# Performance work log

Measured on AMD Instinct MI355X. Metric: run time of the kernel, lower is better.

## Reference

```python
import jax, jax.numpy as jnp
import numpy as np

B, T, C, H = 4, 2048, 1024, 64  # batch, seq, embedding_size, head_size

def setup_inputs() -> dict:
    key = jax.random.key(0)
    k0, k1, k2, k3 = jax.random.split(key, 4)
    scale = 0.02
    return {
        "x":  jax.random.normal(k0, (B, T, C), dtype=jnp.float32),
        "Wq": jax.random.normal(k1, (H, C), dtype=jnp.float32) * scale,
        "Wk": jax.random.normal(k2, (H, C), dtype=jnp.float32) * scale,
        "Wv": jax.random.normal(k3, (H, C), dtype=jnp.float32) * scale,
    }

def reference(x, Wq, Wk, Wv):
    # Linear(bias=False): y = x @ W^T
    q = jnp.einsum('btc,hc->bth', x, Wq)
    k = jnp.einsum('btc,hc->bth', x, Wk)
    v = jnp.einsum('btc,hc->bth', x, Wv)
    # NOTE: original scales by embedding_size C**-0.5, not head_size
    wei = jnp.einsum('bth,bsh->bts', q, k) * (x.shape[-1] ** -0.5)
    t = x.shape[1]
    causal_mask = jnp.tril(jnp.ones((t, t), dtype=bool))  # [T, T]
    wei = jnp.where(causal_mask, wei, -jnp.inf)
    wei = jax.nn.softmax(wei, axis=-1)
    # dropout = 0.0 -> identity (eval mode)
    out = jnp.einsum('bts,bsh->bth', wei, v)
    return out
```

## Files before the change

### kernel.cpp

```cpp
#include <hip/hip_runtime.h>
#include <hip/hip_bf16.h>

typedef unsigned short u16;
typedef __attribute__((ext_vector_type(8))) __bf16 bf16x8;
typedef __attribute__((ext_vector_type(4))) float f32x4;

#define B_ 4
#define T_ 2048
#define C_ 1024
#define H_ 64
#define NSEG 8

__device__ __forceinline__ u16 f2bf(float f) {
    union { __hip_bfloat16 h; u16 u; } cv;
    cv.h = __float2bfloat16(f);
    return cv.u;
}

__device__ __forceinline__ bf16x8 cvt8r(float4 f0, float4 f1) {
    union { u16 h[8]; bf16x8 v; } ua;
    ua.h[0] = f2bf(f0.x); ua.h[1] = f2bf(f0.y);
    ua.h[2] = f2bf(f0.z); ua.h[3] = f2bf(f0.w);
    ua.h[4] = f2bf(f1.x); ua.h[5] = f2bf(f1.y);
    ua.h[6] = f2bf(f1.z); ua.h[7] = f2bf(f1.w);
    return ua.v;
}

__device__ __forceinline__ void gll16(const void* g, void* l) {
    __builtin_amdgcn_global_load_lds(
        (const __attribute__((address_space(1))) void*)g,
        (__attribute__((address_space(3))) void*)l, 16, 0, 0);
}

__global__ __launch_bounds__(256) void wpack(
    const float* __restrict__ wq, const float* __restrict__ wk,
    const float* __restrict__ wv, u16* __restrict__ wP)
{
    int u    = blockIdx.x * 256 + threadIdx.x;
    int ln   = u & 63;
    int frag = u >> 6;
    int ksg  = frag & 31;
    int j16  = frag >> 5;
    int n    = j16 * 16 + (ln & 15);
    int kb   = ksg * 32 + (ln >> 4) * 8;
    const float* src = (n < 64) ? (wq + (size_t)n * C_)
                     : (n < 128) ? (wk + (size_t)(n - 64) * C_)
                                 : (wv + (size_t)(n - 128) * C_);
    float4 f0 = *(const float4*)(src + kb);
    float4 f1 = *(const float4*)(src + kb + 4);
    *(bf16x8*)(wP + (size_t)u * 8) = cvt8r(f0, f1);
}

__global__ __launch_bounds__(512) void qkv(
    const float* __restrict__ x, const u16* __restrict__ wP,
    u16* __restrict__ qP, u16* __restrict__ kP, u16* __restrict__ vP)
{
    __shared__ __align__(16) char smem[32768];

    const int tid = threadIdx.x;
    const int ln  = tid & 63;
    const int w   = tid >> 6;
    const int m0  = blockIdx.x * 32;

    const int lr = ln & 15;
    const int g  = ln >> 4;
    const int ms = w >> 2;
    const int nh = w & 3;

    f32x4 acc[3] = {};

    const int xrow = w * 4 + (ln >> 4);
    const int xc   = (ln & 15) ^ (xrow & 7);

#define STAGE(BUF, KC)                                                     \
    gll16(x + (size_t)(m0 + xrow) * C_ + (KC) * 64 + xc * 4,               \
          smem + (BUF) * 8192 + w * 1024)

    STAGE(0, 0);
    STAGE(1, 1);
    STAGE(2, 2);

    const int ra  = ms * 16 + lr;
    const int rsw = ra & 7;
    const u16* wbase = wP + (size_t)(nh * 3) * 32 * 64 * 8;

    #pragma unroll
    for (int kc = 0; kc < 16; ++kc) {
        if (kc == 0)       asm volatile("s_waitcnt vmcnt(2)"  ::: "memory");
        else if (kc == 1)  asm volatile("s_waitcnt vmcnt(8)"  ::: "memory");
        else if (kc <= 13) asm volatile("s_waitcnt vmcnt(14)" ::: "memory");
        else if (kc == 14) asm volatile("s_waitcnt vmcnt(13)" ::: "memory");
        else               asm volatile("s_waitcnt vmcnt(12)" ::: "memory");
        __builtin_amdgcn_s_barrier();
        __builtin_amdgcn_sched_barrier(0);

        const char* rb = smem + (kc & 3) * 8192;

        bf16x8 a[2];
        #pragma unroll
        for (int ks = 0; ks < 2; ++ks) {
            int c0 = ks * 8 + g * 2;
            float4 fa = *(const float4*)(rb + ra * 256 + ((c0       ^ rsw) << 4));
            float4 fb = *(const float4*)(rb + ra * 256 + (((c0 + 1) ^ rsw) << 4));
            a[ks] = cvt8r(fa, fb);
        }

        #pragma unroll
        for (int j = 0; j < 3; ++j) {
            #pragma unroll
            for (int ks = 0; ks < 2; ++ks) {
                size_t fragofs = ((size_t)(j * 32 + kc * 2 + ks) * 64 + ln) * 8;
                bf16x8 b = *(const bf16x8*)(wbase + fragofs);
                acc[j] = __builtin_amdgcn_mfma_f32_16x16x32_bf16(a[ks], b, acc[j], 0, 0, 0);
            }
        }

        if (kc < 13) STAGE((kc + 3) & 3, kc + 3);
    }
#undef STAGE

    __syncthreads();

    float* tile = (float*)smem;
    #pragma unroll
    for (int j = 0; j < 3; ++j)
        #pragma unroll
        for (int i = 0; i < 4; ++i)
            tile[(ms * 16 + g * 4 + i) * 201 + nh * 48 + j * 16 + lr] = acc[j][i];
    __syncthreads();

    for (int uu = tid; uu < 768; uu += 512) {
        const int ln2 = uu & 63;
        const int lr2 = ln2 & 15;
        const int g2  = ln2 >> 4;
        if (uu < 512) {
            const int isK = uu >> 8;
            const int rem = uu & 255;
            const int u   = rem >> 7;
            const int ks  = (rem >> 6) & 1;
            const float* src = tile + (u * 16 + lr2) * 201 + isK * 64 + ks * 32 + g2 * 8;
            float4 f0 = *(const float4*)src;
            float4 f1 = *(const float4*)(src + 4);
            bf16x8 val = cvt8r(f0, f1);
            u16* dst = (isK ? kP : qP)
                     + ((size_t)(((m0 >> 4) + u) * 2 + ks) * 64 + ln2) * 8;
            *(bf16x8*)dst = val;
        } else {
            const int rem = uu - 512;
            const int jf  = rem >> 6;
            union { u16 h[8]; bf16x8 v; } ua;
            #pragma unroll
            for (int e = 0; e < 8; ++e)
                ua.h[e] = f2bf(tile[(g2 * 8 + e) * 201 + 128 + jf * 16 + lr2]);
            u16* dst = vP + ((size_t)((m0 >> 5) * 4 + jf) * 64 + ln2) * 8;
            *(bf16x8*)dst = ua.v;
        }
    }
}

__global__ __launch_bounds__(512) void attn(
    const u16* __restrict__ qP, const u16* __restrict__ kP,
    const u16* __restrict__ vP, float* __restrict__ out)
{
    __shared__ __align__(16) char shm[34816];

    const int tid  = threadIdx.x;
    const int lane = tid & 63;
    const int seg  = tid >> 6;
    const int tix  = blockIdx.x;
    const int b    = tix & 3;
    const int qt   = 127 - (tix >> 2);
    const int q0   = qt * 16;

    const int lr = lane & 15;
    const int g  = lane >> 4;
    const int lk = g * 8;

    const int nch = (qt >> 2) + 1;
    const int L   = (nch + NSEG - 1) >> 3;
    const int c0  = seg * L;
    const int c1  = min(nch, c0 + L);

    f32x4 oacc[4] = {};
    float mrow[4], lrow[4];
    #pragma unroll
    for (int i = 0; i < 4; ++i) { mrow[i] = -1e30f; lrow[i] = 0.f; }

    if (c0 < c1) {
        bf16x8 aq[2];
        #pragma unroll
        for (int ks = 0; ks < 2; ++ks)
            aq[ks] = *(const bf16x8*)(qP + ((size_t)((b * 128 + qt) * 2 + ks) * 64 + lane) * 8);

        u16* myps = (u16*)shm + seg * 1152;

        for (int jc = c0; jc < c1; ++jc) {
            const int kv0 = jc << 6;

            bf16x8 bk[8];
            #pragma unroll
            for (int jf = 0; jf < 4; ++jf)
                #pragma unroll
                for (int ks = 0; ks < 2; ++ks)
                    bk[jf * 2 + ks] = *(const bf16x8*)(kP +
                        ((size_t)((b * 128 + (kv0 >> 4) + jf) * 2 + ks) * 64 + lane) * 8);

            f32x4 sacc[4] = {};
            #pragma unroll
            for (int jf = 0; jf < 4; ++jf)
                #pragma unroll
                for (int ks = 0; ks < 2; ++ks)
                    sacc[jf] = __builtin_amdgcn_mfma_f32_16x16x32_bf16(aq[ks], bk[jf * 2 + ks], sacc[jf], 0, 0, 0);

            bf16x8 bv[8];
            #pragma unroll
            for (int ks2 = 0; ks2 < 2; ++ks2)
                #pragma unroll
                for (int jf = 0; jf < 4; ++jf)
                    bv[jf * 2 + ks2] = *(const bf16x8*)(vP +
                        ((size_t)((b * 64 + (kv0 >> 5) + ks2) * 4 + jf) * 64 + lane) * 8);

            const bool full = (kv0 + 63 <= q0);
            #pragma unroll
            for (int jf = 0; jf < 4; ++jf) {
                int col = kv0 + jf * 16 + lr;
                #pragma unroll
                for (int i = 0; i < 4; ++i) {
                    int row = q0 + g * 4 + i;
                    float val = sacc[jf][i] * 0.03125f;
                    sacc[jf][i] = (full || col <= row) ? val : -1e30f;
                }
            }

            float pnew[4][4];
            #pragma unroll
            for (int i = 0; i < 4; ++i) {
                float mx = fmaxf(fmaxf(sacc[0][i], sacc[1][i]), fmaxf(sacc[2][i], sacc[3][i]));
                mx = fmaxf(mx, __shfl_xor(mx, 1));
                mx = fmaxf(mx, __shfl_xor(mx, 2));
                mx = fmaxf(mx, __shfl_xor(mx, 4));
                mx = fmaxf(mx, __shfl_xor(mx, 8));
                float mnew = fmaxf(mrow[i], mx);
                float corr = __expf(mrow[i] - mnew);
                float rs = 0.f;
                #pragma unroll
                for (int jf = 0; jf < 4; ++jf) {
                    float p = __expf(sacc[jf][i] - mnew);
                    pnew[jf][i] = p;
                    rs += p;
                }
                rs += __shfl_xor(rs, 1);
                rs += __shfl_xor(rs, 2);
                rs += __shfl_xor(rs, 4);
                rs += __shfl_xor(rs, 8);
                lrow[i] = lrow[i] * corr + rs;
                mrow[i] = mnew;
                #pragma unroll
                for (int jf = 0; jf < 4; ++jf) oacc[jf][i] *= corr;
            }

            #pragma unroll
            for (int jf = 0; jf < 4; ++jf)
                #pragma unroll
                for (int i = 0; i < 4; ++i)
                    myps[(g * 4 + i) * 72 + jf * 16 + lr] = f2bf(pnew[jf][i]);

            #pragma unroll
            for (int ks2 = 0; ks2 < 2; ++ks2) {
                bf16x8 ap = *(const bf16x8*)(myps + lr * 72 + ks2 * 32 + lk);
                #pragma unroll
                for (int jf = 0; jf < 4; ++jf)
                    oacc[jf] = __builtin_amdgcn_mfma_f32_16x16x32_bf16(ap, bv[jf * 2 + ks2], oacc[jf], 0, 0, 0);
            }
        }
    }

    __syncthreads();

    float* part = (float*)shm;
    float* mlp  = part + 8 * 16 * 66;

    if (c0 >= c1) {
        if (lr == 0)
            #pragma unroll
            for (int i = 0; i < 4; ++i) {
                mlp[(seg * 16 + g * 4 + i) * 2]     = -1e30f;
                mlp[(seg * 16 + g * 4 + i) * 2 + 1] = 0.f;
            }
    } else {
        #pragma unroll
        for (int jf = 0; jf < 4; ++jf)
            #pragma unroll
            for (int i = 0; i < 4; ++i)
                part[(seg * 16 + g * 4 + i) * 66 + jf * 16 + lr] = oacc[jf][i];
        if (lr == 0)
            #pragma unroll
            for (int i = 0; i < 4; ++i) {
                mlp[(seg * 16 + g * 4 + i) * 2]     = mrow[i];
                mlp[(seg * 16 + g * 4 + i) * 2 + 1] = lrow[i];
            }
    }

    __syncthreads();

    if (tid < 256) {
        const int row = tid >> 4;
        const int p   = tid & 15;

        float m2[NSEG], l2[NSEG];
        #pragma unroll
        for (int s = 0; s < NSEG; ++s) {
            m2[s] = mlp[(s * 16 + row) * 2];
            l2[s] = mlp[(s * 16 + row) * 2 + 1];
        }
        float M = m2[0];
        #pragma unroll
        for (int s = 1; s < NSEG; ++s) M = fmaxf(M, m2[s]);

        float a0 = 0.f, a1 = 0.f, a2 = 0.f, a3 = 0.f, Lsum = 0.f;
        #pragma unroll
        for (int s = 0; s < NSEG; ++s) {
            if (l2[s] != 0.f) {
                float wgt = __expf(m2[s] - M);
                Lsum += l2[s] * wgt;
                const float* pp = part + (s * 16 + row) * 66 + p * 4;
                a0 += wgt * pp[0];
                a1 += wgt * pp[1];
                a2 += wgt * pp[2];
                a3 += wgt * pp[3];
            }
        }
        float inv = 1.f / Lsum;
        float4 r; r.x = a0 * inv; r.y = a1 * inv; r.z = a2 * inv; r.w = a3 * inv;
        *(float4*)(out + ((size_t)b * T_ + qt * 16 + row) * H_ + p * 4) = r;
    }
}

extern "C" void kernel_launch(void* const* d_in, const int* in_sizes, int n_in,
                              void* d_out, int out_size, void* d_ws, size_t ws_size,
                              hipStream_t stream) {
    const float* x  = (const float*)d_in[0];
    const float* wq = (const float*)d_in[1];
    const float* wk = (const float*)d_in[2];
    const float* wv = (const float*)d_in[3];

    u16* qPws = (u16*)d_ws;
    u16* kPws = qPws + (size_t)B_ * T_ * H_;
    u16* vPws = kPws + (size_t)B_ * T_ * H_;
    u16* wPws = vPws + (size_t)B_ * T_ * H_;

    wpack<<<96, 256, 0, stream>>>(wq, wk, wv, wPws);
    qkv<<<256, 512, 0, stream>>>(x, wPws, qPws, kPws, vPws);
    attn<<<512, 512, 0, stream>>>(qPws, kPws, vPws, (float*)d_out);
}
```

Before: 37.88 us.

## Fuse QKV projection and attention into one kernel with grid-wide barrier

Merges the qkv and attn kernels into a single persistent kernel of 256 blocks. Blocks first compute their QKV tile, then synchronize through a global atomic counter barrier (reset in wpack), and each block then processes two attention tiles (tix and 511-tix) to balance the causal workload. This removes one kernel launch and its tail/drain gap, but adds a spin barrier that assumes all 256 blocks are co-resident and halves the number of attention blocks in flight.

```diff
diff --git a/kernel.cpp b/kernel.cpp
--- a/kernel.cpp
+++ b/kernel.cpp
@@ -10,6 +10,7 @@
 #define C_ 1024
 #define H_ 64
 #define NSEG 8
+#define GRID 256
 
 __device__ __forceinline__ u16 f2bf(float f) {
     union { __hip_bfloat16 h; u16 u; } cv;
@@ -34,8 +35,10 @@
 
 __global__ __launch_bounds__(256) void wpack(
     const float* __restrict__ wq, const float* __restrict__ wk,
-    const float* __restrict__ wv, u16* __restrict__ wP)
+    const float* __restrict__ wv, u16* __restrict__ wP,
+    unsigned* __restrict__ bar)
 {
+    if (blockIdx.x == 0 && threadIdx.x == 0) bar[0] = 0;
     int u    = blockIdx.x * 256 + threadIdx.x;
     int ln   = u & 63;
     int frag = u >> 6;
@@ -51,288 +54,296 @@
     *(bf16x8*)(wP + (size_t)u * 8) = cvt8r(f0, f1);
 }
 
-__global__ __launch_bounds__(512) void qkv(
+__global__ __launch_bounds__(512) void fused(
     const float* __restrict__ x, const u16* __restrict__ wP,
-    u16* __restrict__ qP, u16* __restrict__ kP, u16* __restrict__ vP)
+    u16* __restrict__ qP, u16* __restrict__ kP, u16* __restrict__ vP,
+    float* __restrict__ out, unsigned* __restrict__ bar)
 {
-    __shared__ __align__(16) char smem[32768];
+    __shared__ __align__(16) char shm[34816];
 
     const int tid = threadIdx.x;
     const int ln  = tid & 63;
     const int w   = tid >> 6;
-    const int m0  = blockIdx.x * 32;
-
-    const int lr = ln & 15;
-    const int g  = ln >> 4;
-    const int ms = w >> 2;
-    const int nh = w & 3;
-
-    f32x4 acc[3] = {};
-
-    const int xrow = w * 4 + (ln >> 4);
-    const int xc   = (ln & 15) ^ (xrow & 7);
+    const int lr  = ln & 15;
+    const int g   = ln >> 4;
+    const int lk  = g * 8;
+
+    {
+        char* smem = shm;
+        const int m0 = blockIdx.x * 32;
+        const int ms = w >> 2;
+        const int nh = w & 3;
+
+        f32x4 acc[3] = {};
+
+        const int xrow = w * 4 + (ln >> 4);
+        const int xc   = (ln & 15) ^ (xrow & 7);
 
 #define STAGE(BUF, KC)                                                     \
     gll16(x + (size_t)(m0 + xrow) * C_ + (KC) * 64 + xc * 4,               \
           smem + (BUF) * 8192 + w * 1024)
 
-    STAGE(0, 0);
-    STAGE(1, 1);
-    STAGE(2, 2);
-
-    const int ra  = ms * 16 + lr;
-    const int rsw = ra & 7;
-    const u16* wbase = wP + (size_t)(nh * 3) * 32 * 64 * 8;
-
-    #pragma unroll
-    for (int kc = 0; kc < 16; ++kc) {
-        if (kc == 0)       asm volatile("s_waitcnt vmcnt(2)"  ::: "memory");
-        else if (kc == 1)  asm volatile("s_waitcnt vmcnt(8)"  ::: "memory");
-        else if (kc <= 13) asm volatile("s_waitcnt vmcnt(14)" ::: "memory");
-        else if (kc == 14) asm volatile("s_waitcnt vmcnt(13)" ::: "memory");
-        else               asm volatile("s_waitcnt vmcnt(12)" ::: "memory");
-        __builtin_amdgcn_s_barrier();
-        __builtin_amdgcn_sched_barrier(0);
-
-        const char* rb = smem + (kc & 3) * 8192;
-
-        bf16x8 a[2];
+        STAGE(0, 0);
+        STAGE(1, 1);
+        STAGE(2, 2);
+
+        const int ra  = ms * 16 + lr;
+        const int rsw = ra & 7;
+        const u16* wbase = wP + (size_t)(nh * 3) * 32 * 64 * 8;
+
         #pragma unroll
-        for (int ks = 0; ks < 2; ++ks) {
-            int c0 = ks * 8 + g * 2;
-            float4 fa = *(const float4*)(rb + ra * 256 + ((c0       ^ rsw) << 4));
-            float4 fb = *(const float4*)(rb + ra * 256 + (((c0 + 1) ^ rsw) << 4));
-            a[ks] = cvt8r(fa, fb);
-        }
-
+        for (int kc = 0; kc < 16; ++kc) {
+            if (kc == 0)       asm volatile("s_waitcnt vmcnt(2)"  ::: "memory");
+            else if (kc == 1)  asm volatile("s_waitcnt vmcnt(8)"  ::: "memory");
+            else if (kc <= 13) asm volatile("s_waitcnt vmcnt(14)" ::: "memory");
+            else if (kc == 14) asm volatile("s_waitcnt vmcnt(13)" ::: "memory");
+            else               asm volatile("s_waitcnt vmcnt(12)" ::: "memory");
+            __builtin_amdgcn_s_barrier();
+            __builtin_amdgcn_sched_barrier(0);
+
+            const char* rb = smem + (kc & 3) * 8192;
+
+            bf16x8 a[2];
+            #pragma unroll
+            for (int ks = 0; ks < 2; ++ks) {
+                int c0 = ks * 8 + g * 2;
+                float4 fa = *(const float4*)(rb + ra * 256 + ((c0       ^ rsw) << 4));
+                float4 fb = *(const float4*)(rb + ra * 256 + (((c0 + 1) ^ rsw) << 4));
+                a[ks] = cvt8r(fa, fb);
+            }
+
+            #pragma unroll
+            for (int j = 0; j < 3; ++j) {
+                #pragma unroll
+                for (int ks = 0; ks < 2; ++ks) {
+                    size_t fragofs = ((size_t)(j * 32 + kc * 2 + ks) * 64 + ln) * 8;
+                    bf16x8 b = *(const bf16x8*)(wbase + fragofs);
+                    acc[j] = __builtin_amdgcn_mfma_f32_16x16x32_bf16(a[ks], b, acc[j], 0, 0, 0);
+                }
+            }
+
+            if (kc < 13) STAGE((kc + 3) & 3, kc + 3);
+        }
+#undef STAGE
+
+        __syncthreads();
+
+        float* tile = (float*)smem;
         #pragma unroll
-        for (int j = 0; j < 3; ++j) {
-            #pragma unroll
-            for (int ks = 0; ks < 2; ++ks) {
-                size_t fragofs = ((size_t)(j * 32 + kc * 2 + ks) * 64 + ln) * 8;
-                bf16x8 b = *(const bf16x8*)(wbase + fragofs);
-                acc[j] = __builtin_amdgcn_mfma_f32_16x16x32_bf16(a[ks], b, acc[j], 0, 0, 0);
-            }
-        }
-
-        if (kc < 13) STAGE((kc + 3) & 3, kc + 3);
+        for (int j = 0; j < 3; ++j)
+            #pragma unroll
+            for (int i = 0; i < 4; ++i)
+                tile[(ms * 16 + g * 4 + i) * 201 + nh * 48 + j * 16 + lr] = acc[j][i];
+        __syncthreads();
+
+        for (int uu = tid; uu < 768; uu += 512) {
+            const int ln2 = uu & 63;
+            const int lr2 = ln2 & 15;
+            const int g2  = ln2 >> 4;
+            if (uu < 512) {
+                const int isK = uu >> 8;
+                const int rem = uu & 255;
+                const int u   = rem >> 7;
+                const int ks  = (rem >> 6) & 1;
+                const float* src = tile + (u * 16 + lr2) * 201 + isK * 64 + ks * 32 + g2 * 8;
+                float4 f0 = *(const float4*)src;
+                float4 f1 = *(const float4*)(src + 4);
+                bf16x8 val = cvt8r(f0, f1);
+                u16* dst = (isK ? kP : qP)
+                         + ((size_t)(((m0 >> 4) + u) * 2 + ks) * 64 + ln2) * 8;
+                *(bf16x8*)dst = val;
+            } else {
+                const int rem = uu - 512;
+                const int jf  = rem >> 6;
+                union { u16 h[8]; bf16x8 v; } ua;
+                #pragma unroll
+                for (int e = 0; e < 8; ++e)
+                    ua.h[e] = f2bf(tile[(g2 * 8 + e) * 201 + 128 + jf * 16 + lr2]);
+                u16* dst = vP + ((size_t)((m0 >> 5) * 4 + jf) * 64 + ln2) * 8;
+                *(bf16x8*)dst = ua.v;
+            }
+        }
     }
-#undef STAGE
 
     __syncthreads();
-
-    float* tile = (float*)smem;
-    #pragma unroll
-    for (int j = 0; j < 3; ++j)
+    if (tid == 0) {
+        __threadfence();
+        atomicAdd(bar, 1u);
+        while (__hip_atomic_load(bar, __ATOMIC_RELAXED, __HIP_MEMORY_SCOPE_AGENT) < GRID)
+            __builtin_amdgcn_s_sleep(2);
+        __threadfence();
+    }
+    __syncthreads();
+
+    const int seg = w;
+
+    #pragma unroll 1
+    for (int t2 = 0; t2 < 2; ++t2) {
+        const int tix = (t2 == 0) ? blockIdx.x : (511 - blockIdx.x);
+        const int b   = tix & 3;
+        const int qt  = 127 - (tix >> 2);
+        const int q0  = qt * 16;
+
+        const int nch = (qt >> 2) + 1;
+        const int L   = (nch + NSEG - 1) >> 3;
+        const int c0  = seg * L;
+        const int c1  = min(nch, c0 + L);
+
+        f32x4 oacc[4] = {};
+        float mrow[4], lrow[4];
         #pragma unroll
-        for (int i = 0; i < 4; ++i)
-            tile[(ms * 16 + g * 4 + i) * 201 + nh * 48 + j * 16 + lr] = acc[j][i];
-    __syncthreads();
-
-    for (int uu = tid; uu < 768; uu += 512) {
-        const int ln2 = uu & 63;
-        const int lr2 = ln2 & 15;
-        const int g2  = ln2 >> 4;
-        if (uu < 512) {
-            const int isK = uu >> 8;
-            const int rem = uu & 255;
-            const int u   = rem >> 7;
-            const int ks  = (rem >> 6) & 1;
-            const float* src = tile + (u * 16 + lr2) * 201 + isK * 64 + ks * 32 + g2 * 8;
-            float4 f0 = *(const float4*)src;
-            float4 f1 = *(const float4*)(src + 4);
-            bf16x8 val = cvt8r(f0, f1);
-            u16* dst = (isK ? kP : qP)
-                     + ((size_t)(((m0 >> 4) + u) * 2 + ks) * 64 + ln2) * 8;
-            *(bf16x8*)dst = val;
+        for (int i = 0; i < 4; ++i) { mrow[i] = -1e30f; lrow[i] = 0.f; }
+
+        if (c0 < c1) {
+            bf16x8 aq[2];
+            #pragma unroll
+            for (int ks = 0; ks < 2; ++ks)
+                aq[ks] = *(const bf16x8*)(qP + ((size_t)((b * 128 + qt) * 2 + ks) * 64 + ln) * 8);
+
+            u16* myps = (u16*)shm + seg * 1152;
+
+            for (int jc = c0; jc < c1; ++jc) {
+                const int kv0 = jc << 6;
+
+                bf16x8 bk[8];
+                #pragma unroll
+                for (int jf = 0; jf < 4; ++jf)
+                    #pragma unroll
+                    for (int ks = 0; ks < 2; ++ks)
+                        bk[jf * 2 + ks] = *(const bf16x8*)(kP +
+                            ((size_t)((b * 128 + (kv0 >> 4) + jf) * 2 + ks) * 64 + ln) * 8);
+
+                f32x4 sacc[4] = {};
+                #pragma unroll
+                for (int jf = 0; jf < 4; ++jf)
+                    #pragma unroll
+                    for (int ks = 0; ks < 2; ++ks)
+                        sacc[jf] = __builtin_amdgcn_mfma_f32_16x16x32_bf16(aq[ks], bk[jf * 2 + ks], sacc[jf], 0, 0, 0);
+
+                bf16x8 bv[8];
+                #pragma unroll
+                for (int ks2 = 0; ks2 < 2; ++ks2)
+                    #pragma unroll
+                    for (int jf = 0; jf < 4; ++jf)
+                        bv[jf * 2 + ks2] = *(const bf16x8*)(vP +
+                            ((size_t)((b * 64 + (kv0 >> 5) + ks2) * 4 + jf) * 64 + ln) * 8);
+
+                const bool full = (kv0 + 63 <= q0);
+                #pragma unroll
+                for (int jf = 0; jf < 4; ++jf) {
+                    int col = kv0 + jf * 16 + lr;
+                    #pragma unroll
+                    for (int i = 0; i < 4; ++i) {
+                        int row = q0 + g * 4 + i;
+                        float val = sacc[jf][i] * 0.03125f;
+                        sacc[jf][i] = (full || col <= row) ? val : -1e30f;
+                    }
+                }
+
+                float pnew[4][4];
+                #pragma unroll
+                for (int i = 0; i < 4; ++i) {
+                    float mx = fmaxf(fmaxf(sacc[0][i], sacc[1][i]), fmaxf(sacc[2][i], sacc[3][i]));
+                    mx = fmaxf(mx, __shfl_xor(mx, 1));
+                    mx = fmaxf(mx, __shfl_xor(mx, 2));
+                    mx = fmaxf(mx, __shfl_xor(mx, 4));
+                    mx = fmaxf(mx, __shfl_xor(mx, 8));
+                    float mnew = fmaxf(mrow[i], mx);
+                    float corr = __expf(mrow[i] - mnew);
+                    float rs = 0.f;
+                    #pragma unroll
+                    for (int jf = 0; jf < 4; ++jf) {
+                        float p = __expf(sacc[jf][i] - mnew);
+                        pnew[jf][i] = p;
+                        rs += p;
+                    }
+                    rs += __shfl_xor(rs, 1);
+                    rs += __shfl_xor(rs, 2);
+                    rs += __shfl_xor(rs, 4);
+                    rs += __shfl_xor(rs, 8);
+                    lrow[i] = lrow[i] * corr + rs;
+                    mrow[i] = mnew;
+                    #pragma unroll
+                    for (int jf = 0; jf < 4; ++jf) oacc[jf][i] *= corr;
+                }
+
+                #pragma unroll
+                for (int jf = 0; jf < 4; ++jf)
+                    #pragma unroll
+                    for (int i = 0; i < 4; ++i)
+                        myps[(g * 4 + i) * 72 + jf * 16 + lr] = f2bf(pnew[jf][i]);
+
+                #pragma unroll
+                for (int ks2 = 0; ks2 < 2; ++ks2) {
+                    bf16x8 ap = *(const bf16x8*)(myps + lr * 72 + ks2 * 32 + lk);
+                    #pragma unroll
+                    for (int jf = 0; jf < 4; ++jf)
+                        oacc[jf] = __builtin_amdgcn_mfma_f32_16x16x32_bf16(ap, bv[jf * 2 + ks2], oacc[jf], 0, 0, 0);
+                }
+            }
+        }
+
+        __syncthreads();
+
+        float* part = (float*)shm;
+        float* mlp  = part + 8 * 16 * 66;
+
+        if (c0 >= c1) {
+            if (lr == 0)
+                #pragma unroll
+                for (int i = 0; i < 4; ++i) {
+                    mlp[(seg * 16 + g * 4 + i) * 2]     = -1e30f;
+                    mlp[(seg * 16 + g * 4 + i) * 2 + 1] = 0.f;
+                }
         } else {
-            const int rem = uu - 512;
-            const int jf  = rem >> 6;
-            union { u16 h[8]; bf16x8 v; } ua;
-            #pragma unroll
-            for (int e = 0; e < 8; ++e)
-                ua.h[e] = f2bf(tile[(g2 * 8 + e) * 201 + 128 + jf * 16 + lr2]);
-            u16* dst = vP + ((size_t)((m0 >> 5) * 4 + jf) * 64 + ln2) * 8;
-            *(bf16x8*)dst = ua.v;
-        }
-    }
-}
-
-__global__ __launch_bounds__(512) void attn(
-    const u16* __restrict__ qP, const u16* __restrict__ kP,
-    const u16* __restrict__ vP, float* __restrict__ out)
-{
-    __shared__ __align__(16) char shm[34816];
-
-    const int tid  = threadIdx.x;
-    const int lane = tid & 63;
-    const int seg  = tid >> 6;
-    const int tix  = blockIdx.x;
-    const int b    = tix & 3;
-    const int qt   = 127 - (tix >> 2);
-    const int q0   = qt * 16;
-
-    const int lr = lane & 15;
-    const int g  = lane >> 4;
-    const int lk = g * 8;
-
-    const int nch = (qt >> 2) + 1;
-    const int L   = (nch + NSEG - 1) >> 3;
-    const int c0  = seg * L;
-    const int c1  = min(nch, c0 + L);
-
-    f32x4 oacc[4] = {};
-    float mrow[4], lrow[4];
-    #pragma unroll
-    for (int i = 0; i < 4; ++i) { mrow[i] = -1e30f; lrow[i] = 0.f; }
-
-    if (c0 < c1) {
-        bf16x8 aq[2];
-        #pragma unroll
-        for (int ks = 0; ks < 2; ++ks)
-            aq[ks] = *(const bf16x8*)(qP + ((size_t)((b * 128 + qt) * 2 + ks) * 64 + lane) * 8);
-
-        u16* myps = (u16*)shm + seg * 1152;
-
-        for (int jc = c0; jc < c1; ++jc) {
-            const int kv0 = jc << 6;
-
-            bf16x8 bk[8];
             #pragma unroll
             for (int jf = 0; jf < 4; ++jf)
                 #pragma unroll
-                for (int ks = 0; ks < 2; ++ks)
-                    bk[jf * 2 + ks] = *(const bf16x8*)(kP +
-                        ((size_t)((b * 128 + (kv0 >> 4) + jf) * 2 + ks) * 64 + lane) * 8);
-
-            f32x4 sacc[4] = {};
-            #pragma unroll
-            for (int jf = 0; jf < 4; ++jf)
-                #pragma unroll
-                for (int ks = 0; ks < 2; ++ks)
-                    sacc[jf] = __builtin_amdgcn_mfma_f32_16x16x32_bf16(aq[ks], bk[jf * 2 + ks], sacc[jf], 0, 0, 0);
-
-            bf16x8 bv[8];
-            #pragma unroll
-            for (int ks2 = 0; ks2 < 2; ++ks2)
-                #pragma unroll
-                for (int jf = 0; jf < 4; ++jf)
-                    bv[jf * 2 + ks2] = *(const bf16x8*)(vP +
-                        ((size_t)((b * 64 + (kv0 >> 5) + ks2) * 4 + jf) * 64 + lane) * 8);
-
-            const bool full = (kv0 + 63 <= q0);
-            #pragma unroll
-            for (int jf = 0; jf < 4; ++jf) {
-                int col = kv0 + jf * 16 + lr;
+                for (int i = 0; i < 4; ++i)
+                    part[(seg * 16 + g * 4 + i) * 66 + jf * 16 + lr] = oacc[jf][i];
+            if (lr == 0)
                 #pragma unroll
                 for (int i = 0; i < 4; ++i) {
-                    int row = q0 + g * 4 + i;
-                    float val = sacc[jf][i] * 0.03125f;
-                    sacc[jf][i] = (full || col <= row) ? val : -1e30f;
-                }
-            }
-
-            float pnew[4][4];
-            #pragma unroll
-            for (int i = 0; i < 4; ++i) {
-                float mx = fmaxf(fmaxf(sacc[0][i], sacc[1][i]), fmaxf(sacc[2][i], sacc[3][i]));
-                mx = fmaxf(mx, __shfl_xor(mx, 1));
-                mx = fmaxf(mx, __shfl_xor(mx, 2));
-                mx = fmaxf(mx, __shfl_xor(mx, 4));
-                mx = fmaxf(mx, __shfl_xor(mx, 8));
-                float mnew = fmaxf(mrow[i], mx);
-                float corr = __expf(mrow[i] - mnew);
-                float rs = 0.f;
-                #pragma unroll
-                for (int jf = 0; jf < 4; ++jf) {
-                    float p = __expf(sacc[jf][i] - mnew);
-                    pnew[jf][i] = p;
-                    rs += p;
-                }
-                rs += __shfl_xor(rs, 1);
-                rs += __shfl_xor(rs, 2);
-                rs += __shfl_xor(rs, 4);
-                rs += __shfl_xor(rs, 8);
-                lrow[i] = lrow[i] * corr + rs;
-                mrow[i] = mnew;
-                #pragma unroll
-                for (int jf = 0; jf < 4; ++jf) oacc[jf][i] *= corr;
-            }
-
-            #pragma unroll
-            for (int jf = 0; jf < 4; ++jf)
-                #pragma unroll
-                for (int i = 0; i < 4; ++i)
-                    myps[(g * 4 + i) * 72 + jf * 16 + lr] = f2bf(pnew[jf][i]);
-
-            #pragma unroll
-            for (int ks2 = 0; ks2 < 2; ++ks2) {
-                bf16x8 ap = *(const bf16x8*)(myps + lr * 72 + ks2 * 32 + lk);
-                #pragma unroll
-                for (int jf = 0; jf < 4; ++jf)
-                    oacc[jf] = __builtin_amdgcn_mfma_f32_16x16x32_bf16(ap, bv[jf * 2 + ks2], oacc[jf], 0, 0, 0);
-            }
-        }
-    }
-
-    __syncthreads();
-
-    float* part = (float*)shm;
-    float* mlp  = part + 8 * 16 * 66;
-
-    if (c0 >= c1) {
-        if (lr == 0)
-            #pragma unroll
-            for (int i = 0; i < 4; ++i) {
-                mlp[(seg * 16 + g * 4 + i) * 2]     = -1e30f;
-                mlp[(seg * 16 + g * 4 + i) * 2 + 1] = 0.f;
-            }
-    } else {
-        #pragma unroll
-        for (int jf = 0; jf < 4; ++jf)
-            #pragma unroll
-            for (int i = 0; i < 4; ++i)
-                part[(seg * 16 + g * 4 + i) * 66 + jf * 16 + lr] = oacc[jf][i];
-        if (lr == 0)
-            #pragma unroll
-            for (int i = 0; i < 4; ++i) {
-                mlp[(seg * 16 + g * 4 + i) * 2]     = mrow[i];
-                mlp[(seg * 16 + g * 4 + i) * 2 + 1] = lrow[i];
-            }
-    }
-
-    __syncthreads();
-
-    if (tid < 256) {
-        const int row = tid >> 4;
-        const int p   = tid & 15;
-
-        float m2[NSEG], l2[NSEG];
-        #pragma unroll
-        for (int s = 0; s < NSEG; ++s) {
-            m2[s] = mlp[(s * 16 + row) * 2];
-            l2[s] = mlp[(s * 16 + row) * 2 + 1];
-        }
-        float M = m2[0];
-        #pragma unroll
-        for (int s = 1; s < NSEG; ++s) M = fmaxf(M, m2[s]);
-
-        float a0 = 0.f, a1 = 0.f, a2 = 0.f, a3 = 0.f, Lsum = 0.f;
-        #pragma unroll
-        for (int s = 0; s < NSEG; ++s) {
-            if (l2[s] != 0.f) {
-                float wgt = __expf(m2[s] - M);
-                Lsum += l2[s] * wgt;
-                const float* pp = part + (s * 16 + row) * 66 + p * 4;
-                a0 += wgt * pp[0];
-                a1 += wgt * pp[1];
-                a2 += wgt * pp[2];
-                a3 += wgt * pp[3];
-            }
-        }
-        float inv = 1.f / Lsum;
-        float4 r; r.x = a0 * inv; r.y = a1 * inv; r.z = a2 * inv; r.w = a3 * inv;
-        *(float4*)(out + ((size_t)b * T_ + qt * 16 + row) * H_ + p * 4) = r;
+                    mlp[(seg * 16 + g * 4 + i) * 2]     = mrow[i];
+                    mlp[(seg * 16 + g * 4 + i) * 2 + 1] = lrow[i];
+                }
+        }
+
+        __syncthreads();
+
+        if (tid < 256) {
+            const int row = tid >> 4;
+            const int p   = tid & 15;
+
+            float m2[NSEG], l2[NSEG];
+            #pragma unroll
+            for (int s = 0; s < NSEG; ++s) {
+                m2[s] = mlp[(s * 16 + row) * 2];
+                l2[s] = mlp[(s * 16 + row) * 2 + 1];
+            }
+            float M = m2[0];
+            #pragma unroll
+            for (int s = 1; s < NSEG; ++s) M = fmaxf(M, m2[s]);
+
+            float a0 = 0.f, a1 = 0.f, a2 = 0.f, a3 = 0.f, Lsum = 0.f;
+            #pragma unroll
+            for (int s = 0; s < NSEG; ++s) {
+                if (l2[s] != 0.f) {
+                    float wgt = __expf(m2[s] - M);
+                    Lsum += l2[s] * wgt;
+                    const float* pp = part + (s * 16 + row) * 66 + p * 4;
+                    a0 += wgt * pp[0];
+                    a1 += wgt * pp[1];
+                    a2 += wgt * pp[2];
+                    a3 += wgt * pp[3];
+                }
+            }
+            float inv = 1.f / Lsum;
+            float4 r; r.x = a0 * inv; r.y = a1 * inv; r.z = a2 * inv; r.w = a3 * inv;
+            *(float4*)(out + ((size_t)b * T_ + qt * 16 + row) * H_ + p * 4) = r;
+        }
+
+        __syncthreads();
     }
 }
 
@@ -344,12 +355,12 @@
     const float* wk = (const float*)d_in[2];
     const float* wv = (const float*)d_in[3];
 
-    u16* qPws = (u16*)d_ws;
+    unsigned* bar = (unsigned*)d_ws;
+    u16* qPws = (u16*)((char*)d_ws + 256);
     u16* kPws = qPws + (size_t)B_ * T_ * H_;
     u16* vPws = kPws + (size_t)B_ * T_ * H_;
     u16* wPws = vPws + (size_t)B_ * T_ * H_;
 
-    wpack<<<96, 256, 0, stream>>>(wq, wk, wv, wPws);
-    qkv<<<256, 512, 0, stream>>>(x, wPws, qPws, kPws, vPws);
-    attn<<<512, 512, 0, stream>>>(qPws, kPws, vPws, (float*)d_out);
-}
+    wpack<<<96, 256, 0, stream>>>(wq, wk, wv, wPws, bar);
+    fused<<<GRID, 512, 0, stream>>>(x, wPws, qPws, kPws, vPws, (float*)d_out, bar);
+}
```

Result: slower. 57.99 us (+53.1%).
